# Kernel tuning notes

Measured on AMD Instinct MI355X. Metric: run time of the kernel, lower is better.

Reference implementation:

```python
import jax, jax.numpy as jnp
import numpy as np

ROT_ERR_W = 15.0   # weight[0]
TRANS_ERR_W = 100.0  # weight[1]
CONV_ROT = 0.0
CONV_TRANS = 0.0
EPS = 1e-7
SMALL = 1e-4


def _skew(w):
    # w: [..., 3] -> [..., 3, 3]
    z = jnp.zeros_like(w[..., 0])
    r0 = jnp.stack([z, -w[..., 2], w[..., 1]], axis=-1)
    r1 = jnp.stack([w[..., 2], z, -w[..., 0]], axis=-1)
    r2 = jnp.stack([-w[..., 1], w[..., 0], z], axis=-1)
    return jnp.stack([r0, r1, r2], axis=-2)


def _log_se3(R, t):
    # SE(3) log map. R: [...,3,3], t: [...,3] -> (theta, omega[...,3], v[...,3])
    tr = R[..., 0, 0] + R[..., 1, 1] + R[..., 2, 2]
    cos_t = jnp.clip((tr - 1.0) * 0.5, -1.0 + EPS, 1.0 - EPS)
    theta = jnp.arccos(cos_t)
    sin_t = jnp.sin(theta)
    # vee(R - R^T)/2
    w_vee = 0.5 * jnp.stack([
        R[..., 2, 1] - R[..., 1, 2],
        R[..., 0, 2] - R[..., 2, 0],
        R[..., 1, 0] - R[..., 0, 1],
    ], axis=-1)
    small = theta < SMALL
    safe_sin = jnp.where(small, 1.0, sin_t)
    scale = jnp.where(small, 1.0 + theta * theta / 6.0, theta / safe_sin)
    omega = scale[..., None] * w_vee
    # V^{-1} t -> translational twist
    wx = _skew(omega)
    wx2 = jnp.matmul(wx, wx)
    theta2 = jnp.where(small, 1.0, theta * theta)
    A = jnp.where(
        small,
        jnp.full_like(theta, 1.0 / 12.0),
        (1.0 - (theta * sin_t) / (2.0 * (1.0 - cos_t))) / theta2,
    )
    Vinv = jnp.eye(3, dtype=R.dtype) - 0.5 * wx + A[..., None, None] * wx2
    v = jnp.einsum('...ij,...j->...i', Vinv, t)
    return theta, omega, v


def setup_inputs() -> dict:
    key = jax.random.key(0)
    k1, k2, k3, k4 = jax.random.split(key, 4)
    B, H = 2048, 2048  # n_particles x horizon
    return {
        'ee_pos_batch': jax.random.normal(k1, (B, H, 3), jnp.float32),
        'ee_rot_batch': jax.random.normal(k2, (B, H, 3, 3), jnp.float32),
        'ee_goal_pos': jax.random.normal(k3, (3,), jnp.float32),
        'ee_goal_rot': jax.random.normal(k4, (3, 3), jnp.float32),
        'vec_weight': jnp.ones((6,), jnp.float32),
    }


def reference(ee_pos_batch, ee_rot_batch, ee_goal_pos, ee_goal_rot, vec_weight):
    # goal_to_ee = inverse(ee_to_world) * goal_to_world
    Rt = jnp.swapaxes(ee_rot_batch, -1, -2)                 # R_ee^T, [B,H,3,3]
    R_ge = jnp.matmul(Rt, ee_goal_rot)                       # [B,H,3,3]
    t_ge = jnp.einsum('bhij,bhj->bhi', Rt, ee_goal_pos - ee_pos_batch)
    _, omega, v = _log_se3(R_ge, t_ge)
    # squared_l2 NormCost with unit weight
    position_err = jnp.sum(jnp.square(vec_weight[3:6] * v), axis=-1)
    rotation_err = jnp.sum(jnp.square(vec_weight[0:3] * omega), axis=-1)
    rotation_err = jnp.where(rotation_err < CONV_ROT, 0.0, rotation_err)
    position_err = jnp.where(position_err < CONV_TRANS, 0.0, position_err)
    cost = ROT_ERR_W * rotation_err + TRANS_ERR_W * position_err
    return cost, rotation_err, position_err, v, omega
```

## Files before the change

kernel.cpp:

```cpp
#include <hip/hip_runtime.h>


#define BLOCK 256

__global__ __launch_bounds__(BLOCK) void pose_cost_kernel(
    const float* __restrict__ pos,
    const float* __restrict__ rot,
    const float* __restrict__ gpos,
    const float* __restrict__ grot,
    const float* __restrict__ wvec,
    float* __restrict__ out,
    int N)
{
    __shared__ float sR[BLOCK * 9];
    __shared__ float sP[BLOCK * 3];

    const int t = threadIdx.x;
    const int base = blockIdx.x * BLOCK;
    const bool fullBlock = (base + BLOCK) <= N;

    {
        const float* rsrc = rot + (size_t)base * 9;
        const float* psrc = pos + (size_t)base * 3;
        if (fullBlock) {
            #pragma unroll
            for (int k = 0; k < 9; ++k) sR[k * BLOCK + t] = rsrc[k * BLOCK + t];
            #pragma unroll
            for (int k = 0; k < 3; ++k) sP[k * BLOCK + t] = psrc[k * BLOCK + t];
        } else {
            int rem = N - base;
            #pragma unroll
            for (int k = 0; k < 9; ++k) {
                int i = k * BLOCK + t;
                if (i < rem * 9) sR[i] = rsrc[i];
            }
            #pragma unroll
            for (int k = 0; k < 3; ++k) {
                int i = k * BLOCK + t;
                if (i < rem * 3) sP[i] = psrc[i];
            }
        }
    }

    float G[9], g0, g1, g2, w[6];
    #pragma unroll
    for (int k = 0; k < 9; ++k) G[k] = grot[k];
    g0 = gpos[0]; g1 = gpos[1]; g2 = gpos[2];
    #pragma unroll
    for (int k = 0; k < 6; ++k) w[k] = wvec[k];

    __syncthreads();

    const int idx = base + t;
    const bool active = idx < N;

    float cost = 0.f, re = 0.f, pe = 0.f;
    float v0 = 0.f, v1 = 0.f, v2 = 0.f, o0 = 0.f, o1 = 0.f, o2 = 0.f;

    if (active) {
        float R[9];
        #pragma unroll
        for (int k = 0; k < 9; ++k) R[k] = sR[t * 9 + k];
        const float p0 = sP[t * 3 + 0];
        const float p1 = sP[t * 3 + 1];
        const float p2 = sP[t * 3 + 2];

        const float d0 = g0 - p0, d1 = g1 - p1, d2 = g2 - p2;
        const float tq0 = R[0] * d0 + R[3] * d1 + R[6] * d2;
        const float tq1 = R[1] * d0 + R[4] * d1 + R[7] * d2;
        const float tq2 = R[2] * d0 + R[5] * d1 + R[8] * d2;

        float M[9];
        #pragma unroll
        for (int i = 0; i < 3; ++i) {
            #pragma unroll
            for (int j = 0; j < 3; ++j) {
                M[i * 3 + j] = R[0 + i] * G[0 + j] + R[3 + i] * G[3 + j] + R[6 + i] * G[6 + j];
            }
        }

        const float tr = M[0] + M[4] + M[8];
        float cos_t = (tr - 1.0f) * 0.5f;
        cos_t = fminf(fmaxf(cos_t, -1.0f + 1e-7f), 1.0f - 1e-7f);
        const float theta = acosf(cos_t);
        const float sin_t = sinf(theta);

        const float wv0 = 0.5f * (M[7] - M[5]);
        const float wv1 = 0.5f * (M[2] - M[6]);
        const float wv2 = 0.5f * (M[3] - M[1]);

        const bool small = theta < 1e-4f;
        const float th2 = theta * theta;
        const float scale = small ? (1.0f + th2 * (1.0f / 6.0f)) : (theta / sin_t);
        o0 = scale * wv0; o1 = scale * wv1; o2 = scale * wv2;

        const float theta2 = small ? 1.0f : th2;
        const float A = small ? (1.0f / 12.0f)
                              : (1.0f - (theta * sin_t) / (2.0f * (1.0f - cos_t))) / theta2;

        const float cx0 = o1 * tq2 - o2 * tq1;
        const float cx1 = o2 * tq0 - o0 * tq2;
        const float cx2 = o0 * tq1 - o1 * tq0;
        const float odt = o0 * tq0 + o1 * tq1 + o2 * tq2;
        const float on2 = o0 * o0 + o1 * o1 + o2 * o2;
        v0 = tq0 - 0.5f * cx0 + A * (o0 * odt - on2 * tq0);
        v1 = tq1 - 0.5f * cx1 + A * (o1 * odt - on2 * tq1);
        v2 = tq2 - 0.5f * cx2 + A * (o2 * odt - on2 * tq2);

        const float we0 = w[0] * o0, we1 = w[1] * o1, we2 = w[2] * o2;
        const float wp0 = w[3] * v0, wp1 = w[4] * v1, wp2 = w[5] * v2;
        re = we0 * we0 + we1 * we1 + we2 * we2;
        pe = wp0 * wp0 + wp1 * wp1 + wp2 * wp2;
        re = (re < 0.0f) ? 0.0f : re;
        pe = (pe < 0.0f) ? 0.0f : pe;
        cost = 15.0f * re + 100.0f * pe;

        out[idx] = cost;
        out[(size_t)N + idx] = re;
        out[2 * (size_t)N + idx] = pe;
    }

    __syncthreads();
    if (active) {
        sR[t * 3 + 0] = v0;
        sR[t * 3 + 1] = v1;
        sR[t * 3 + 2] = v2;
        sR[BLOCK * 3 + t * 3 + 0] = o0;
        sR[BLOCK * 3 + t * 3 + 1] = o1;
        sR[BLOCK * 3 + t * 3 + 2] = o2;
    }
    __syncthreads();

    {
        float* vdst = out + 3 * (size_t)N + (size_t)base * 3;
        float* odst = out + 6 * (size_t)N + (size_t)base * 3;
        if (fullBlock) {
            #pragma unroll
            for (int k = 0; k < 3; ++k) vdst[k * BLOCK + t] = sR[k * BLOCK + t];
            #pragma unroll
            for (int k = 0; k < 3; ++k) odst[k * BLOCK + t] = sR[BLOCK * 3 + k * BLOCK + t];
        } else {
            int rem = N - base;
            #pragma unroll
            for (int k = 0; k < 3; ++k) {
                int i = k * BLOCK + t;
                if (i < rem * 3) { vdst[i] = sR[i]; odst[i] = sR[BLOCK * 3 + i]; }
            }
        }
    }
}

extern "C" void kernel_launch(void* const* d_in, const int* in_sizes, int n_in,
                              void* d_out, int out_size, void* d_ws, size_t ws_size,
                              hipStream_t stream) {
    const float* pos  = (const float*)d_in[0];
    const float* rot  = (const float*)d_in[1];
    const float* gpos = (const float*)d_in[2];
    const float* grot = (const float*)d_in[3];
    const float* wv   = (const float*)d_in[4];
    float* out = (float*)d_out;

    const int N = in_sizes[0] / 3;
    const int blocks = (N + BLOCK - 1) / BLOCK;
    hipLaunchKernelGGL(pose_cost_kernel, dim3(blocks), dim3(BLOCK), 0, stream,
                       pos, rot, gpos, grot, wv, out, N);
}
```

Measured before the change: 295.5 us.

## Process four poses per thread with 128-bit vector loads and stores, no LDS staging

```diff
diff --git a/kernel.cpp b/kernel.cpp
--- a/kernel.cpp
+++ b/kernel.cpp
@@ -2,6 +2,63 @@
 
 
 #define BLOCK 256
+
+typedef float f32x4 __attribute__((ext_vector_type(4)));
+
+__device__ __forceinline__ void pose_one(
+    const float* R, float p0, float p1, float p2,
+    const float* G, float g0, float g1, float g2, const float* w,
+    float& cost, float& re, float& pe,
+    float& v0, float& v1, float& v2,
+    float& o0, float& o1, float& o2)
+{
+    const float d0 = g0 - p0, d1 = g1 - p1, d2 = g2 - p2;
+    const float tq0 = R[0] * d0 + R[3] * d1 + R[6] * d2;
+    const float tq1 = R[1] * d0 + R[4] * d1 + R[7] * d2;
+    const float tq2 = R[2] * d0 + R[5] * d1 + R[8] * d2;
+
+    float M[9];
+    #pragma unroll
+    for (int i = 0; i < 3; ++i)
+        #pragma unroll
+        for (int j = 0; j < 3; ++j)
+            M[i * 3 + j] = R[0 + i] * G[0 + j] + R[3 + i] * G[3 + j] + R[6 + i] * G[6 + j];
+
+    const float tr = M[0] + M[4] + M[8];
+    float cos_t = (tr - 1.0f) * 0.5f;
+    cos_t = fminf(fmaxf(cos_t, -1.0f + 1e-7f), 1.0f - 1e-7f);
+    const float theta = acosf(cos_t);
+    const float sin_t = sqrtf(fmaf(-cos_t, cos_t, 1.0f));
+
+    const float wv0 = 0.5f * (M[7] - M[5]);
+    const float wv1 = 0.5f * (M[2] - M[6]);
+    const float wv2 = 0.5f * (M[3] - M[1]);
+
+    const bool small = theta < 1e-4f;
+    const float th2 = theta * theta;
+    const float scale = small ? (1.0f + th2 * (1.0f / 6.0f)) : (theta / sin_t);
+    o0 = scale * wv0; o1 = scale * wv1; o2 = scale * wv2;
+
+    const float A = small ? (1.0f / 12.0f)
+                          : (1.0f - 0.5f * scale * (1.0f + cos_t)) / th2;
+
+    const float cx0 = o1 * tq2 - o2 * tq1;
+    const float cx1 = o2 * tq0 - o0 * tq2;
+    const float cx2 = o0 * tq1 - o1 * tq0;
+    const float odt = o0 * tq0 + o1 * tq1 + o2 * tq2;
+    const float on2 = o0 * o0 + o1 * o1 + o2 * o2;
+    v0 = tq0 - 0.5f * cx0 + A * (o0 * odt - on2 * tq0);
+    v1 = tq1 - 0.5f * cx1 + A * (o1 * odt - on2 * tq1);
+    v2 = tq2 - 0.5f * cx2 + A * (o2 * odt - on2 * tq2);
+
+    const float we0 = w[0] * o0, we1 = w[1] * o1, we2 = w[2] * o2;
+    const float wp0 = w[3] * v0, wp1 = w[4] * v1, wp2 = w[5] * v2;
+    re = we0 * we0 + we1 * we1 + we2 * we2;
+    pe = wp0 * wp0 + wp1 * wp1 + wp2 * wp2;
+    re = (re < 0.0f) ? 0.0f : re;
+    pe = (pe < 0.0f) ? 0.0f : pe;
+    cost = 15.0f * re + 100.0f * pe;
+}
 
 __global__ __launch_bounds__(BLOCK) void pose_cost_kernel(
     const float* __restrict__ pos,
@@ -12,140 +69,89 @@
     float* __restrict__ out,
     int N)
 {
-    __shared__ float sR[BLOCK * 9];
-    __shared__ float sP[BLOCK * 3];
+    const size_t tid = (size_t)blockIdx.x * BLOCK + threadIdx.x;
+    const size_t i0 = tid * 4;
+    if (i0 >= (size_t)N) return;
 
-    const int t = threadIdx.x;
-    const int base = blockIdx.x * BLOCK;
-    const bool fullBlock = (base + BLOCK) <= N;
-
-    {
-        const float* rsrc = rot + (size_t)base * 9;
-        const float* psrc = pos + (size_t)base * 3;
-        if (fullBlock) {
-            #pragma unroll
-            for (int k = 0; k < 9; ++k) sR[k * BLOCK + t] = rsrc[k * BLOCK + t];
-            #pragma unroll
-            for (int k = 0; k < 3; ++k) sP[k * BLOCK + t] = psrc[k * BLOCK + t];
-        } else {
-            int rem = N - base;
-            #pragma unroll
-            for (int k = 0; k < 9; ++k) {
-                int i = k * BLOCK + t;
-                if (i < rem * 9) sR[i] = rsrc[i];
-            }
-            #pragma unroll
-            for (int k = 0; k < 3; ++k) {
-                int i = k * BLOCK + t;
-                if (i < rem * 3) sP[i] = psrc[i];
-            }
-        }
-    }
-
-    float G[9], g0, g1, g2, w[6];
+    float G[9], w[6];
     #pragma unroll
     for (int k = 0; k < 9; ++k) G[k] = grot[k];
-    g0 = gpos[0]; g1 = gpos[1]; g2 = gpos[2];
+    const float g0 = gpos[0], g1 = gpos[1], g2 = gpos[2];
     #pragma unroll
     for (int k = 0; k < 6; ++k) w[k] = wvec[k];
 
-    __syncthreads();
+    const size_t Ns = (size_t)N;
 
-    const int idx = base + t;
-    const bool active = idx < N;
+    if (((N & 3) == 0)) {
+        const f32x4* rs = reinterpret_cast<const f32x4*>(rot + i0 * 9);
+        const f32x4* ps = reinterpret_cast<const f32x4*>(pos + i0 * 3);
+        f32x4 r[9], p[3];
+        #pragma unroll
+        for (int k = 0; k < 9; ++k) r[k] = rs[k];
+        #pragma unroll
+        for (int k = 0; k < 3; ++k) p[k] = ps[k];
 
-    float cost = 0.f, re = 0.f, pe = 0.f;
-    float v0 = 0.f, v1 = 0.f, v2 = 0.f, o0 = 0.f, o1 = 0.f, o2 = 0.f;
+        #define RF(q) (r[(q) >> 2][(q) & 3])
+        #define PF(q) (p[(q) >> 2][(q) & 3])
 
-    if (active) {
-        float R[9];
+        f32x4 vcost, vre, vpe;
+        f32x4 vv[3], vo[3];
+        #define VV(q) (vv[(q) >> 2][(q) & 3])
+        #define VO(q) (vo[(q) >> 2][(q) & 3])
+
         #pragma unroll
-        for (int k = 0; k < 9; ++k) R[k] = sR[t * 9 + k];
-        const float p0 = sP[t * 3 + 0];
-        const float p1 = sP[t * 3 + 1];
-        const float p2 = sP[t * 3 + 2];
+        for (int j = 0; j < 4; ++j) {
+            float R[9];
+            #pragma unroll
+            for (int k = 0; k < 9; ++k) R[k] = RF(9 * j + k);
+            const float p0 = PF(3 * j + 0);
+            const float p1 = PF(3 * j + 1);
+            const float p2 = PF(3 * j + 2);
 
-        const float d0 = g0 - p0, d1 = g1 - p1, d2 = g2 - p2;
-        const float tq0 = R[0] * d0 + R[3] * d1 + R[6] * d2;
-        const float tq1 = R[1] * d0 + R[4] * d1 + R[7] * d2;
-        const float tq2 = R[2] * d0 + R[5] * d1 + R[8] * d2;
+            float c, re, pe, v0, v1, v2, o0, o1, o2;
+            pose_one(R, p0, p1, p2, G, g0, g1, g2, w,
+                     c, re, pe, v0, v1, v2, o0, o1, o2);
+            vcost[j] = c; vre[j] = re; vpe[j] = pe;
+            VV(3 * j + 0) = v0; VV(3 * j + 1) = v1; VV(3 * j + 2) = v2;
+            VO(3 * j + 0) = o0; VO(3 * j + 1) = o1; VO(3 * j + 2) = o2;
+        }
+        #undef RF
+        #undef PF
+        #undef VV
+        #undef VO
 
-        float M[9];
+        *reinterpret_cast<f32x4*>(out + i0) = vcost;
+        *reinterpret_cast<f32x4*>(out + Ns + i0) = vre;
+        *reinterpret_cast<f32x4*>(out + 2 * Ns + i0) = vpe;
+        f32x4* vd = reinterpret_cast<f32x4*>(out + 3 * Ns + i0 * 3);
+        f32x4* od = reinterpret_cast<f32x4*>(out + 6 * Ns + i0 * 3);
         #pragma unroll
-        for (int i = 0; i < 3; ++i) {
+        for (int k = 0; k < 3; ++k) vd[k] = vv[k];
+        #pragma unroll
+        for (int k = 0; k < 3; ++k) od[k] = vo[k];
+    } else {
+        const size_t iend = (i0 + 4 < Ns) ? (i0 + 4) : Ns;
+        for (size_t i = i0; i < iend; ++i) {
+            float R[9];
             #pragma unroll
-            for (int j = 0; j < 3; ++j) {
-                M[i * 3 + j] = R[0 + i] * G[0 + j] + R[3 + i] * G[3 + j] + R[6 + i] * G[6 + j];
-            }
-        }
+            for (int k = 0; k < 9; ++k) R[k] = rot[i * 9 + k];
+            const float p0 = pos[i * 3 + 0];
+            const float p1 = pos[i * 3 + 1];
+            const float p2 = pos[i * 3 + 2];
 
-        const float tr = M[0] + M[4] + M[8];
-        float cos_t = (tr - 1.0f) * 0.5f;
-        cos_t = fminf(fmaxf(cos_t, -1.0f + 1e-7f), 1.0f - 1e-7f);
-        const float theta = acosf(cos_t);
-        const float sin_t = sinf(theta);
+            float c, re, pe, v0, v1, v2, o0, o1, o2;
+            pose_one(R, p0, p1, p2, G, g0, g1, g2, w,
+                     c, re, pe, v0, v1, v2, o0, o1, o2);
 
-        const float wv0 = 0.5f * (M[7] - M[5]);
-        const float wv1 = 0.5f * (M[2] - M[6]);
-        const float wv2 = 0.5f * (M[3] - M[1]);
-
-        const bool small = theta < 1e-4f;
-        const float th2 = theta * theta;
-        const float scale = small ? (1.0f + th2 * (1.0f / 6.0f)) : (theta / sin_t);
-        o0 = scale * wv0; o1 = scale * wv1; o2 = scale * wv2;
-
-        const float theta2 = small ? 1.0f : th2;
-        const float A = small ? (1.0f / 12.0f)
-                              : (1.0f - (theta * sin_t) / (2.0f * (1.0f - cos_t))) / theta2;
-
-        const float cx0 = o1 * tq2 - o2 * tq1;
-        const float cx1 = o2 * tq0 - o0 * tq2;
-        const float cx2 = o0 * tq1 - o1 * tq0;
-        const float odt = o0 * tq0 + o1 * tq1 + o2 * tq2;
-        const float on2 = o0 * o0 + o1 * o1 + o2 * o2;
-        v0 = tq0 - 0.5f * cx0 + A * (o0 * odt - on2 * tq0);
-        v1 = tq1 - 0.5f * cx1 + A * (o1 * odt - on2 * tq1);
-        v2 = tq2 - 0.5f * cx2 + A * (o2 * odt - on2 * tq2);
-
-        const float we0 = w[0] * o0, we1 = w[1] * o1, we2 = w[2] * o2;
-        const float wp0 = w[3] * v0, wp1 = w[4] * v1, wp2 = w[5] * v2;
-        re = we0 * we0 + we1 * we1 + we2 * we2;
-        pe = wp0 * wp0 + wp1 * wp1 + wp2 * wp2;
-        re = (re < 0.0f) ? 0.0f : re;
-        pe = (pe < 0.0f) ? 0.0f : pe;
-        cost = 15.0f * re + 100.0f * pe;
-
-        out[idx] = cost;
-        out[(size_t)N + idx] = re;
-        out[2 * (size_t)N + idx] = pe;
-    }
-
-    __syncthreads();
-    if (active) {
-        sR[t * 3 + 0] = v0;
-        sR[t * 3 + 1] = v1;
-        sR[t * 3 + 2] = v2;
-        sR[BLOCK * 3 + t * 3 + 0] = o0;
-        sR[BLOCK * 3 + t * 3 + 1] = o1;
-        sR[BLOCK * 3 + t * 3 + 2] = o2;
-    }
-    __syncthreads();
-
-    {
-        float* vdst = out + 3 * (size_t)N + (size_t)base * 3;
-        float* odst = out + 6 * (size_t)N + (size_t)base * 3;
-        if (fullBlock) {
-            #pragma unroll
-            for (int k = 0; k < 3; ++k) vdst[k * BLOCK + t] = sR[k * BLOCK + t];
-            #pragma unroll
-            for (int k = 0; k < 3; ++k) odst[k * BLOCK + t] = sR[BLOCK * 3 + k * BLOCK + t];
-        } else {
-            int rem = N - base;
-            #pragma unroll
-            for (int k = 0; k < 3; ++k) {
-                int i = k * BLOCK + t;
-                if (i < rem * 3) { vdst[i] = sR[i]; odst[i] = sR[BLOCK * 3 + i]; }
-            }
+            out[i] = c;
+            out[Ns + i] = re;
+            out[2 * Ns + i] = pe;
+            out[3 * Ns + i * 3 + 0] = v0;
+            out[3 * Ns + i * 3 + 1] = v1;
+            out[3 * Ns + i * 3 + 2] = v2;
+            out[6 * Ns + i * 3 + 0] = o0;
+            out[6 * Ns + i * 3 + 1] = o1;
+            out[6 * Ns + i * 3 + 2] = o2;
         }
     }
 }
@@ -161,7 +167,8 @@
     float* out = (float*)d_out;
 
     const int N = in_sizes[0] / 3;
-    const int blocks = (N + BLOCK - 1) / BLOCK;
+    const int nthreads = (N + 3) / 4;
+    const int blocks = (nthreads + BLOCK - 1) / BLOCK;
     hipLaunchKernelGGL(pose_cost_kernel, dim3(blocks), dim3(BLOCK), 0, stream,
                        pos, rot, gpos, grot, wv, out, N);
 }
```

After: 296.2 us (median of 2 runs). No clear change (+0.3%).
